# Performance work log

Hardware: AMD Instinct MI355X
Metric: run time of the kernel (lower is better)

## Reference

```python
import jax, jax.numpy as jnp
import numpy as np

B, S, D, H = 4, 2048, 256, 8
HD = D // H
SCALE = float(np.sqrt(HD))  # temperature = head_dim ** 0.5


def setup_inputs() -> dict:
    key = jax.random.key(0)
    ks = jax.random.split(key, 12)
    w = lambda k, shape: jax.random.normal(k, shape, dtype=jnp.float32) * 0.05
    x = jax.random.normal(ks[0], (B, S, D), dtype=jnp.float32)
    adj = jax.random.randint(ks[1], (B, S, S), 0, 2, dtype=jnp.int32)
    return {
        "x": x,
        "adj": adj,
        "w_qkv": w(ks[2], (3 * D, D)),
        "b_qkv": jnp.zeros((3 * D,), jnp.float32),
        "ln_g": jnp.ones((D,), jnp.float32),
        "ln_b": jnp.zeros((D,), jnp.float32),
        "w_fc": w(ks[3], (D, D)),
        "b_fc": jnp.zeros((D,), jnp.float32),
        "w_z": w(ks[4], (D, D)),
        "b_z": jnp.full((D,), -2.0, jnp.float32),  # init_bias fills w_z bias with -2
        "u_z": w(ks[5], (D, D)),
        "w_r": w(ks[6], (D, D)),
        "u_r": w(ks[7], (D, D)),
        "w_g": w(ks[8], (D, D)),
        "u_g": w(ks[9], (D, D)),
    }


def reference(x, adj, w_qkv, b_qkv, ln_g, ln_b, w_fc, b_fc,
              w_z, b_z, u_z, w_r, u_r, w_g, u_g):
    residual = x
    # LayerNorm (eps=1e-5, torch default)
    mu = jnp.mean(x, axis=-1, keepdims=True)
    var = jnp.var(x, axis=-1, keepdims=True)
    xn = (x - mu) / jnp.sqrt(var + 1e-5) * ln_g + ln_b
    # fused QKV projection -> (B*H, S, 3*HD), batch-major over (b, h)
    qkv = xn @ w_qkv.T + b_qkv                       # [B,S,3D]
    qkv = qkv.reshape(B, S, H, 3 * HD).transpose(0, 2, 1, 3).reshape(B * H, S, 3 * HD)
    q, k, v = jnp.split(qkv, 3, axis=-1)
    # masked scaled dot-product attention (full NxN scores, as in original)
    attn = jnp.einsum('nqd,nkd->nqk', q, k) / SCALE  # [B*H,S,S]
    adj_r = jnp.repeat(adj, H, axis=0)               # batch-major, matches attn layout
    attn = jnp.where(adj_r == 0, -jnp.inf, attn)
    attn = jax.nn.softmax(attn, axis=-1)
    out = jnp.einsum('nqk,nkd->nqd', attn, v)        # [B*H,S,HD]
    # Faithful replication of torch's view(n_head, batch, ...) applied to
    # batch-major data (an ordering quirk in the original module).
    out = out.reshape(H, B, S, HD).transpose(1, 2, 0, 3).reshape(B, S, D)
    y = jax.nn.relu(out @ w_fc.T + b_fc)
    # GRU gate: x=residual, y=attention branch
    z = jax.nn.sigmoid(y @ w_z.T + b_z + residual @ u_z.T)
    r = jax.nn.sigmoid(y @ w_r.T + residual @ u_r.T)
    h_hat = jnp.tanh(y @ w_g.T + (r * residual) @ u_g.T)
    return (1.0 - z) * residual + z * h_hat
```

## Files before the change

### kernel.cpp

```cpp
#include <hip/hip_runtime.h>
#include <hip/hip_bf16.h>
#include <math.h>

#define B_  4
#define S_  2048
#define D_  256
#define H_  8
#define HD_ 32
#define INV_SCALE 0.17677669529663687f

typedef short  bf16x8 __attribute__((ext_vector_type(8)));
typedef float  f32x4  __attribute__((ext_vector_type(4)));
typedef unsigned short ushort_t;
typedef unsigned int   uint_t;

__device__ __forceinline__ ushort_t f2b(float f) {
    union { float f; unsigned u; } v; v.f = f;
    unsigned r = (v.u + 0x7FFFu + ((v.u >> 16) & 1u)) >> 16;
    return (ushort_t)r;
}
__device__ __forceinline__ float b2f(ushort_t s) {
    return __uint_as_float((uint_t)s << 16);
}

__device__ __forceinline__ float wave_sum(float v) {
#pragma unroll
    for (int o = 32; o > 0; o >>= 1) v += __shfl_down(v, o, 64);
    return v;
}
__device__ __forceinline__ float block_sum256(float v, float* scr) {
    v = wave_sum(v);
    int lane = threadIdx.x & 63, wid = threadIdx.x >> 6;
    if (lane == 0) scr[wid] = v;
    __syncthreads();
    float r = scr[0] + scr[1] + scr[2] + scr[3];
    __syncthreads();
    return r;
}

#define WQ_SZ 196608
#define WS_SZ 65536
#define NB_ADJ 65536
#define NB_WC  2560
#define NB_LN  8192
__global__ __launch_bounds__(256)
void prep_kernel(const int* __restrict__ adj, uint_t* __restrict__ bits,
                 const float* __restrict__ w0, const float* __restrict__ w1,
                 const float* __restrict__ w2, const float* __restrict__ w3,
                 const float* __restrict__ w4, const float* __restrict__ w5,
                 const float* __restrict__ w6, const float* __restrict__ w7,
                 ushort_t* __restrict__ wout,
                 const float* __restrict__ x, const float* __restrict__ g,
                 const float* __restrict__ bb, ushort_t* __restrict__ xn_b) {
    __shared__ float scr[4];
    int blk = blockIdx.x, tid = threadIdx.x;
    if (blk < NB_ADJ) {
        size_t i = (size_t)blk * 256 + tid;
        unsigned long long m = __ballot(adj[i] != 0);
        int lane = tid & 63;
        size_t wbase = ((size_t)blk * 256 + (tid & ~63)) >> 5;
        if (lane == 0)  bits[wbase]     = (uint_t)m;
        if (lane == 32) bits[wbase + 1] = (uint_t)(m >> 32);
    } else if (blk < NB_ADJ + NB_WC) {
        int idx = (blk - NB_ADJ) * 256 + tid;
        const float* src; int o;
        if (idx < WQ_SZ) { src = w0; o = idx; }
        else {
            int j = idx - WQ_SZ, seg = j >> 16; o = j & (WS_SZ - 1);
            src = (seg == 0) ? w1 : (seg == 1) ? w2 : (seg == 2) ? w3 :
                  (seg == 3) ? w4 : (seg == 4) ? w5 : (seg == 5) ? w6 : w7;
        }
        int j  = o & 7;
        int l  = (o >> 3) & 15;
        int qd = (o >> 7) & 3;
        int ks = (o >> 9) & 7;
        int ct = o >> 12;
        wout[idx] = f2b(src[(ct * 16 + l) * 256 + ks * 32 + qd * 8 + j]);
    } else {
        size_t base = (size_t)(blk - NB_ADJ - NB_WC) * D_;
        float v  = x[base + tid];
        float mu = block_sum256(v, scr) * (1.0f / D_);
        float d  = v - mu;
        float var = block_sum256(d * d, scr) * (1.0f / D_);
        float rstd = rsqrtf(var + 1e-5f);
        xn_b[base + tid] = f2b(d * rstd * g[tid] + bb[tid]);
    }
}

__global__ __launch_bounds__(256)
void gemm_qkv(const ushort_t* __restrict__ A, const ushort_t* __restrict__ Wf,
              const float* __restrict__ bias, ushort_t* __restrict__ outb) {
    __shared__ ushort_t Sa[64][264];
    int tid = threadIdx.x;
    int wave = tid >> 6, lane = tid & 63, l = lane & 15, quad = lane >> 4;
    int wm = wave >> 1, wn = wave & 1;
    int m0 = blockIdx.y * 64, n0 = blockIdx.x * 64;
    {
        int row = tid >> 2, c0 = (tid & 3) * 64;
        const ushort_t* ap = A + (size_t)(m0 + row) * 256 + c0;
#pragma unroll
        for (int j = 0; j < 8; ++j)
            *(uint4*)&Sa[row][c0 + 8 * j] = ((const uint4*)ap)[j];
    }
    __syncthreads();

    bf16x8 af[2][8];
#pragma unroll
    for (int mt = 0; mt < 2; ++mt)
#pragma unroll
        for (int ks = 0; ks < 8; ++ks)
            af[mt][ks] = *(const bf16x8*)&Sa[wm * 32 + mt * 16 + l][ks * 32 + quad * 8];

    f32x4 acc[2][2];
#pragma unroll
    for (int i = 0; i < 2; ++i)
#pragma unroll
        for (int j = 0; j < 2; ++j) acc[i][j] = (f32x4){0.f, 0.f, 0.f, 0.f};

#pragma unroll
    for (int nt = 0; nt < 2; ++nt) {
        int ct = (n0 >> 4) + wn * 2 + nt;
        bf16x8 wfr[8];
#pragma unroll
        for (int ks = 0; ks < 8; ++ks)
            wfr[ks] = *(const bf16x8*)(Wf + (((size_t)ct * 8 + ks) * 64 + lane) * 8);
#pragma unroll
        for (int ks = 0; ks < 8; ++ks) {
            acc[0][nt] = __builtin_amdgcn_mfma_f32_16x16x32_bf16(af[0][ks], wfr[ks], acc[0][nt], 0, 0, 0);
            acc[1][nt] = __builtin_amdgcn_mfma_f32_16x16x32_bf16(af[1][ks], wfr[ks], acc[1][nt], 0, 0, 0);
        }
    }

    __syncthreads();
    ushort_t* So = &Sa[0][0];
#pragma unroll
    for (int nt = 0; nt < 2; ++nt) {
        int col = wn * 32 + nt * 16 + l;
        int gcol = n0 + col;
        float bv = bias[gcol];
        float qs = ((gcol % 96) < 32) ? INV_SCALE : 1.0f;
#pragma unroll
        for (int mt = 0; mt < 2; ++mt)
#pragma unroll
            for (int r = 0; r < 4; ++r) {
                int row = wm * 32 + mt * 16 + quad * 4 + r;
                So[row * 72 + col] = f2b((acc[mt][nt][r] + bv) * qs);
            }
    }
    __syncthreads();
    {
        int row = tid >> 2, seg = tid & 3;
        uint4 v0 = *(uint4*)&So[row * 72 + seg * 16];
        uint4 v1 = *(uint4*)&So[row * 72 + seg * 16 + 8];
        ushort_t* op = outb + (size_t)(m0 + row) * 768 + n0 + seg * 16;
        ((uint4*)op)[0] = v0;
        ((uint4*)op)[1] = v1;
    }
}

__global__ __launch_bounds__(256)
void fused_gate(const ushort_t* __restrict__ attn_b, const float* __restrict__ xf,
                const ushort_t* __restrict__ wfc, const ushort_t* __restrict__ wz,
                const ushort_t* __restrict__ uz, const ushort_t* __restrict__ wr,
                const ushort_t* __restrict__ ur, const ushort_t* __restrict__ wg,
                const ushort_t* __restrict__ ug, const float* __restrict__ bfc,
                const float* __restrict__ bz, float* __restrict__ out) {
    __shared__ ushort_t Sa[16][264];
    __shared__ ushort_t Sx[16][264];
    __shared__ ushort_t Sy[16][264];
    __shared__ ushort_t St[16][264];
    int tid = threadIdx.x;
    int wave = tid >> 6, lane = tid & 63, l = lane & 15, quad = lane >> 4;
    int m0 = blockIdx.x * 16;
    int colbase = wave * 64;

    {
        int row = tid >> 4, c0 = (tid & 15) * 16;
        const ushort_t* ap = attn_b + (size_t)(m0 + row) * 256 + c0;
        uint4 a0 = ((const uint4*)ap)[0];
        uint4 a1 = ((const uint4*)ap)[1];
        *(uint4*)&Sa[row][c0] = a0;
        *(uint4*)&Sa[row][c0 + 8] = a1;
        const float4* xp = (const float4*)(xf + (size_t)(m0 + row) * 256 + c0);
        float4 f0 = xp[0], f1 = xp[1], f2_ = xp[2], f3 = xp[3];
        union { __hip_bfloat162 h[4]; uint4 u; } p0, p1;
        p0.h[0] = __float22bfloat162_rn(make_float2(f0.x, f0.y));
        p0.h[1] = __float22bfloat162_rn(make_float2(f0.z, f0.w));
        p0.h[2] = __float22bfloat162_rn(make_float2(f1.x, f1.y));
        p0.h[3] = __float22bfloat162_rn(make_float2(f1.z, f1.w));
        p1.h[0] = __float22bfloat162_rn(make_float2(f2_.x, f2_.y));
        p1.h[1] = __float22bfloat162_rn(make_float2(f2_.z, f2_.w));
        p1.h[2] = __float22bfloat162_rn(make_float2(f3.x, f3.y));
        p1.h[3] = __float22bfloat162_rn(make_float2(f3.z, f3.w));
        *(uint4*)&Sx[row][c0]     = p0.u;
        *(uint4*)&Sx[row][c0 + 8] = p1.u;
    }
    __syncthreads();

    {
        bf16x8 af[8];
#pragma unroll
        for (int ks = 0; ks < 8; ++ks)
            af[ks] = *(const bf16x8*)&Sa[l][ks * 32 + quad * 8];
        f32x4 ya[4];
#pragma unroll
        for (int nt = 0; nt < 4; ++nt) ya[nt] = (f32x4){0.f, 0.f, 0.f, 0.f};
#pragma unroll
        for (int nt = 0; nt < 4; ++nt) {
            size_t fb = ((size_t)(wave * 4 + nt) * 8) * 512 + lane * 8;
#pragma unroll
            for (int ks = 0; ks < 8; ++ks) {
                bf16x8 wfr = *(const bf16x8*)(wfc + fb + ks * 512);
                ya[nt] = __builtin_amdgcn_mfma_f32_16x16x32_bf16(af[ks], wfr, ya[nt], 0, 0, 0);
            }
        }
#pragma unroll
        for (int nt = 0; nt < 4; ++nt) {
            int col = colbase + nt * 16 + l;
            float bv = bfc[col];
#pragma unroll
            for (int r = 0; r < 4; ++r)
                Sy[quad * 4 + r][col] = f2b(fmaxf(ya[nt][r] + bv, 0.0f));
        }
    }
    __syncthreads();

    f32x4 az[4], ar[4], ag[4];
#pragma unroll
    for (int nt = 0; nt < 4; ++nt) {
        az[nt] = (f32x4){0.f, 0.f, 0.f, 0.f};
        ar[nt] = (f32x4){0.f, 0.f, 0.f, 0.f};
        ag[nt] = (f32x4){0.f, 0.f, 0.f, 0.f};
    }
#pragma unroll
    for (int nt = 0; nt < 4; ++nt) {
        size_t fb = ((size_t)(wave * 4 + nt) * 8) * 512 + lane * 8;
#pragma unroll
        for (int ks = 0; ks < 8; ++ks) {
            bf16x8 fy = *(const bf16x8*)&Sy[l][ks * 32 + quad * 8];
            bf16x8 fx = *(const bf16x8*)&Sx[l][ks * 32 + quad * 8];
            bf16x8 fz  = *(const bf16x8*)(wz + fb + ks * 512);
            bf16x8 fuz = *(const bf16x8*)(uz + fb + ks * 512);
            bf16x8 fr  = *(const bf16x8*)(wr + fb + ks * 512);
            bf16x8 fur = *(const bf16x8*)(ur + fb + ks * 512);
            bf16x8 fg  = *(const bf16x8*)(wg + fb + ks * 512);
            az[nt] = __builtin_amdgcn_mfma_f32_16x16x32_bf16(fy, fz,  az[nt], 0, 0, 0);
            az[nt] = __builtin_amdgcn_mfma_f32_16x16x32_bf16(fx, fuz, az[nt], 0, 0, 0);
            ar[nt] = __builtin_amdgcn_mfma_f32_16x16x32_bf16(fy, fr,  ar[nt], 0, 0, 0);
            ar[nt] = __builtin_amdgcn_mfma_f32_16x16x32_bf16(fx, fur, ar[nt], 0, 0, 0);
            ag[nt] = __builtin_amdgcn_mfma_f32_16x16x32_bf16(fy, fg,  ag[nt], 0, 0, 0);
        }
    }
#pragma unroll
    for (int nt = 0; nt < 4; ++nt) {
        int col = colbase + nt * 16 + l;
        float bzv = bz[col];
#pragma unroll
        for (int r = 0; r < 4; ++r) {
            int row = quad * 4 + r;
            az[nt][r] = 1.0f / (1.0f + __expf(-(az[nt][r] + bzv)));
            float rr  = 1.0f / (1.0f + __expf(-ar[nt][r]));
            St[row][col] = f2b(rr * b2f(Sx[row][col]));
        }
    }
    __syncthreads();

    f32x4 fcc[4];
#pragma unroll
    for (int nt = 0; nt < 4; ++nt) fcc[nt] = (f32x4){0.f, 0.f, 0.f, 0.f};
#pragma unroll
    for (int nt = 0; nt < 4; ++nt) {
        size_t fb = ((size_t)(wave * 4 + nt) * 8) * 512 + lane * 8;
#pragma unroll
        for (int ks = 0; ks < 8; ++ks) {
            bf16x8 ft = *(const bf16x8*)&St[l][ks * 32 + quad * 8];
            bf16x8 fu = *(const bf16x8*)(ug + fb + ks * 512);
            fcc[nt] = __builtin_amdgcn_mfma_f32_16x16x32_bf16(ft, fu, fcc[nt], 0, 0, 0);
        }
    }
#pragma unroll
    for (int nt = 0; nt < 4; ++nt) {
        int col = colbase + nt * 16 + l;
#pragma unroll
        for (int r = 0; r < 4; ++r) {
            int row = quad * 4 + r;
            float v = ag[nt][r] + fcc[nt][r];
            float e = __expf(2.0f * v);
            float h = 1.0f - 2.0f / (e + 1.0f);
            float zz = az[nt][r];
            size_t idx = (size_t)(m0 + row) * 256 + col;
            out[idx] = (1.0f - zz) * xf[idx] + zz * h;
        }
    }
}

__global__ __launch_bounds__(256)
void attn_kernel(const ushort_t* __restrict__ qkvb, const uint_t* __restrict__ abits,
                 ushort_t* __restrict__ attn_b) {
    __shared__ ushort_t Ks[64][40];
    __shared__ ushort_t Vt[32][72];
    __shared__ ushort_t Ps[64][72];
    __shared__ uint_t  ab_sh[64][2];

    int tid = threadIdx.x;
    int wave = tid >> 6, lane = tid & 63, l = lane & 15, quad = lane >> 4;
    int q0 = blockIdx.x * 64;
    int n  = blockIdx.y;
    int b = n >> 3, h = n & 7;
    int bp = n & 3, hp = n >> 2;

    const ushort_t* base = qkvb + (size_t)b * S_ * 768 + h * 96;
    int myq = wave * 16 + l;

    bf16x8 qf = *(const bf16x8*)(base + (size_t)(q0 + myq) * 768 + quad * 8);

    f32x4 oacc[2];
    oacc[0] = (f32x4){0.f, 0.f, 0.f, 0.f};
    oacc[1] = (f32x4){0.f, 0.f, 0.f, 0.f};
    float lsum = 0.0f;

    int skey = tid >> 2, spart = tid & 3;
    int kcol = (spart * 8) ^ (((skey >> 3) & 1) << 3);
    int vcol = skey ^ (spart << 4);

    uint4 kv = *(const uint4*)(base + (size_t)skey * 768 + 32 + spart * 8);
    uint4 vv = *(const uint4*)(base + (size_t)skey * 768 + 64 + spart * 8);
    uint_t aw = 0;
    if (tid < 128)
        aw = abits[((size_t)b * S_ + q0 + (tid >> 1)) * 64 + (tid & 1)];

    for (int k0 = 0; k0 < S_; k0 += 64) {
        uint4 kc = kv, vc = vv; uint_t ac = aw;
        if (k0 + 64 < S_) {
            kv = *(const uint4*)(base + (size_t)(k0 + 64 + skey) * 768 + 32 + spart * 8);
            vv = *(const uint4*)(base + (size_t)(k0 + 64 + skey) * 768 + 64 + spart * 8);
            if (tid < 128)
                aw = abits[((size_t)b * S_ + q0 + (tid >> 1)) * 64 + ((k0 + 64) >> 5) + (tid & 1)];
        }
        __syncthreads();
        *(uint4*)&Ks[skey][kcol] = kc;
        {
            const ushort_t* vs = (const ushort_t*)&vc;
#pragma unroll
            for (int i = 0; i < 8; ++i) Vt[spart * 8 + i][vcol] = vs[i];
        }
        if (tid < 128) ab_sh[tid >> 1][tid & 1] = ac;
        __syncthreads();

        uint_t aw0 = ab_sh[myq][0], aw1 = ab_sh[myq][1];

#pragma unroll
        for (int t4 = 0; t4 < 4; ++t4) {
            bf16x8 kf = *(const bf16x8*)&Ks[t4 * 16 + l][(quad * 8) ^ ((l >> 3) << 3)];
            f32x4 z = (f32x4){0.f, 0.f, 0.f, 0.f};
            f32x4 sc = __builtin_amdgcn_mfma_f32_16x16x32_bf16(kf, qf, z, 0, 0, 0);
            uint_t w = (t4 & 2) ? aw1 : aw0;
            uint_t wq = w >> ((t4 & 1) * 16 + quad * 4);
            float p[4];
#pragma unroll
            for (int r = 0; r < 4; ++r) {
                uint_t mneg = 0u - ((wq >> r) & 1u);
                float e = __expf(sc[r]);
                p[r] = __uint_as_float(__float_as_uint(e) & mneg);
                lsum += p[r];
            }
            union { __hip_bfloat162 b2[2]; uint2 u2; } pk;
            pk.b2[0] = __float22bfloat162_rn(make_float2(p[0], p[1]));
            pk.b2[1] = __float22bfloat162_rn(make_float2(p[2], p[3]));
            *(uint2*)&Ps[myq][t4 * 16 + quad * 4] = pk.u2;
        }

#pragma unroll
        for (int ks = 0; ks < 2; ++ks) {
            bf16x8 pf = *(const bf16x8*)&Ps[wave * 16 + l][ks * 32 + quad * 8];
#pragma unroll
            for (int mt = 0; mt < 2; ++mt) {
                int vc2 = (ks * 32 + quad * 8) ^ ((mt * 2 + (l >> 3)) << 4);
                bf16x8 vf = *(const bf16x8*)&Vt[mt * 16 + l][vc2];
                oacc[mt] = __builtin_amdgcn_mfma_f32_16x16x32_bf16(vf, pf, oacc[mt], 0, 0, 0);
            }
        }
    }

    lsum += __shfl_xor(lsum, 16, 64);
    lsum += __shfl_xor(lsum, 32, 64);
    float linv = 1.0f / lsum;

    __syncthreads();
    ushort_t* Ost = &Ks[0][0];
#pragma unroll
    for (int mt = 0; mt < 2; ++mt)
#pragma unroll
        for (int r = 0; r < 4; ++r)
            Ost[myq * 40 + mt * 16 + quad * 4 + r] = f2b(oacc[mt][r] * linv);
    __syncthreads();
    {
        int q = tid >> 2, part = tid & 3;
        uint4 v = *(uint4*)&Ost[q * 40 + part * 8];
        *(uint4*)&attn_b[((size_t)(bp * S_ + q0 + q)) * 256 + hp * 32 + part * 8] = v;
    }
}

extern "C" void kernel_launch(void* const* d_in, const int* in_sizes, int n_in,
                              void* d_out, int out_size, void* d_ws, size_t ws_size,
                              hipStream_t stream) {
    const float* x     = (const float*)d_in[0];
    const int*   adj   = (const int*)d_in[1];
    const float* w_qkv = (const float*)d_in[2];
    const float* b_qkv = (const float*)d_in[3];
    const float* ln_g  = (const float*)d_in[4];
    const float* ln_b  = (const float*)d_in[5];
    const float* w_fc  = (const float*)d_in[6];
    const float* b_fc  = (const float*)d_in[7];
    const float* w_z   = (const float*)d_in[8];
    const float* b_z   = (const float*)d_in[9];
    const float* u_z   = (const float*)d_in[10];
    const float* w_r   = (const float*)d_in[11];
    const float* u_r   = (const float*)d_in[12];
    const float* w_g   = (const float*)d_in[13];
    const float* u_g   = (const float*)d_in[14];
    float* out = (float*)d_out;

    const size_t TOK  = (size_t)B_ * S_;
    const size_t TOKD = TOK * D_;
    ushort_t* xn_b   = (ushort_t*)d_ws;
    ushort_t* qkv_b  = xn_b + TOKD;
    ushort_t* attn_b = qkv_b + TOK * 768;
    ushort_t* wb     = attn_b + TOKD;
    uint_t*   bits   = (uint_t*)(wb + WQ_SZ + 7 * WS_SZ);

    ushort_t* wq_b  = wb;
    ushort_t* wfc_b = wb + WQ_SZ;
    ushort_t* wz_b  = wfc_b + WS_SZ;
    ushort_t* uz_b  = wz_b + WS_SZ;
    ushort_t* wr_b  = uz_b + WS_SZ;
    ushort_t* ur_b  = wr_b + WS_SZ;
    ushort_t* wg_b  = ur_b + WS_SZ;
    ushort_t* ug_b  = wg_b + WS_SZ;

    prep_kernel<<<NB_ADJ + NB_WC + NB_LN, 256, 0, stream>>>(
        adj, bits, w_qkv, w_fc, w_z, u_z, w_r, u_r, w_g, u_g, wb,
        x, ln_g, ln_b, xn_b);

    gemm_qkv<<<dim3(12, 128), 256, 0, stream>>>(xn_b, wq_b, b_qkv, qkv_b);

    attn_kernel<<<dim3(S_ / 64, B_ * H_), 256, 0, stream>>>(qkv_b, bits, attn_b);

    fused_gate<<<512, 256, 0, stream>>>(
        attn_b, x, wfc_b, wz_b, uz_b, wr_b, ur_b, wg_b, ug_b, b_fc, b_z, out);
}
```

Measured before the change: 247.1 us.

## Pre-transpose V in QKV GEMM, double-buffer attention tiles, fold log2e into Q

The QKV GEMM epilogue now also writes V transposed per head into a separate workspace buffer. The attention kernel can then load V rows with vectorized loads instead of scattering scalar transposes into shared memory. K and V tiles are double-buffered, so each iteration needs one barrier instead of two, and mask bits are read straight from global memory into registers instead of through shared memory. The Q scale now includes log2(e), which lets exp2f replace __expf. The cost is an extra V write in the GEMM epilogue plus an extra barrier there.

After: 248.9 us. About the same (+0.7%).

```diff
diff --git a/kernel.cpp b/kernel.cpp
--- a/kernel.cpp
+++ b/kernel.cpp
@@ -7,7 +7,7 @@
 #define D_  256
 #define H_  8
 #define HD_ 32
-#define INV_SCALE 0.17677669529663687f
+#define QSCALE 0.25504175929589786f
 
 typedef short  bf16x8 __attribute__((ext_vector_type(8)));
 typedef float  f32x4  __attribute__((ext_vector_type(4)));
@@ -89,7 +89,8 @@
 
 __global__ __launch_bounds__(256)
 void gemm_qkv(const ushort_t* __restrict__ A, const ushort_t* __restrict__ Wf,
-              const float* __restrict__ bias, ushort_t* __restrict__ outb) {
+              const float* __restrict__ bias, ushort_t* __restrict__ outb,
+              ushort_t* __restrict__ vT) {
     __shared__ ushort_t Sa[64][264];
     int tid = threadIdx.x;
     int wave = tid >> 6, lane = tid & 63, l = lane & 15, quad = lane >> 4;
@@ -138,7 +139,7 @@
         int col = wn * 32 + nt * 16 + l;
         int gcol = n0 + col;
         float bv = bias[gcol];
-        float qs = ((gcol % 96) < 32) ? INV_SCALE : 1.0f;
+        float qs = ((gcol % 96) < 32) ? QSCALE : 1.0f;
 #pragma unroll
         for (int mt = 0; mt < 2; ++mt)
 #pragma unroll
@@ -155,6 +156,33 @@
         ushort_t* op = outb + (size_t)(m0 + row) * 768 + n0 + seg * 16;
         ((uint4*)op)[0] = v0;
         ((uint4*)op)[1] = v1;
+    }
+
+    int vs = n0 % 96;
+    if (vs != 0) {
+        int vloc = (vs == 64) ? 0 : 32;
+        int h  = (n0 + vloc) / 96;
+        int b  = m0 >> 11;
+        int s0 = m0 & (S_ - 1);
+        ushort_t* vstage = &Sa[0][0] + 8192;
+        {
+            int c = tid & 31, seg = tid >> 5;
+            ushort_t tmp[8];
+#pragma unroll
+            for (int i = 0; i < 8; ++i)
+                tmp[i] = So[(seg * 8 + i) * 72 + vloc + c];
+            uint_t u[4];
+#pragma unroll
+            for (int i = 0; i < 4; ++i)
+                u[i] = (uint_t)tmp[2 * i] | ((uint_t)tmp[2 * i + 1] << 16);
+            *(uint4*)&vstage[c * 72 + seg * 8] = make_uint4(u[0], u[1], u[2], u[3]);
+        }
+        __syncthreads();
+        {
+            int d = tid >> 3, tseg = tid & 7;
+            uint4 v = *(uint4*)&vstage[d * 72 + tseg * 8];
+            *(uint4*)&vT[((size_t)(b * 8 + h) * 32 + d) * S_ + s0 + tseg * 8] = v;
+        }
     }
 }
 
@@ -295,12 +323,11 @@
 }
 
 __global__ __launch_bounds__(256)
-void attn_kernel(const ushort_t* __restrict__ qkvb, const uint_t* __restrict__ abits,
-                 ushort_t* __restrict__ attn_b) {
-    __shared__ ushort_t Ks[64][40];
-    __shared__ ushort_t Vt[32][72];
+void attn_kernel(const ushort_t* __restrict__ qkvb, const ushort_t* __restrict__ vT,
+                 const uint_t* __restrict__ abits, ushort_t* __restrict__ attn_b) {
+    __shared__ ushort_t Ks[2][64][40];
+    __shared__ ushort_t Vt[2][32][72];
     __shared__ ushort_t Ps[64][72];
-    __shared__ uint_t  ab_sh[64][2];
 
     int tid = threadIdx.x;
     int wave = tid >> 6, lane = tid & 63, l = lane & 15, quad = lane >> 4;
@@ -321,37 +348,29 @@
 
     int skey = tid >> 2, spart = tid & 3;
     int kcol = (spart * 8) ^ (((skey >> 3) & 1) << 3);
-    int vcol = skey ^ (spart << 4);
+    int vd = tid >> 3, vk = (tid & 7) * 8;
+    const ushort_t* vptr = vT + ((size_t)n * 32 + vd) * S_ + vk;
+    const uint_t* aptr = abits + ((size_t)b * S_ + q0 + myq) * 64;
 
     uint4 kv = *(const uint4*)(base + (size_t)skey * 768 + 32 + spart * 8);
-    uint4 vv = *(const uint4*)(base + (size_t)skey * 768 + 64 + spart * 8);
-    uint_t aw = 0;
-    if (tid < 128)
-        aw = abits[((size_t)b * S_ + q0 + (tid >> 1)) * 64 + (tid & 1)];
+    uint4 vv = *(const uint4*)(vptr);
+    uint2 aw = *(const uint2*)(aptr);
 
     for (int k0 = 0; k0 < S_; k0 += 64) {
-        uint4 kc = kv, vc = vv; uint_t ac = aw;
+        int cur = (k0 >> 6) & 1;
+        *(uint4*)&Ks[cur][skey][kcol] = kv;
+        *(uint4*)&Vt[cur][vd][vk] = vv;
+        uint_t aw0 = aw.x, aw1 = aw.y;
         if (k0 + 64 < S_) {
             kv = *(const uint4*)(base + (size_t)(k0 + 64 + skey) * 768 + 32 + spart * 8);
-            vv = *(const uint4*)(base + (size_t)(k0 + 64 + skey) * 768 + 64 + spart * 8);
-            if (tid < 128)
-                aw = abits[((size_t)b * S_ + q0 + (tid >> 1)) * 64 + ((k0 + 64) >> 5) + (tid & 1)];
+            vv = *(const uint4*)(vptr + k0 + 64);
+            aw = *(const uint2*)(aptr + ((k0 + 64) >> 5));
         }
         __syncthreads();
-        *(uint4*)&Ks[skey][kcol] = kc;
-        {
-            const ushort_t* vs = (const ushort_t*)&vc;
-#pragma unroll
-            for (int i = 0; i < 8; ++i) Vt[spart * 8 + i][vcol] = vs[i];
-        }
-        if (tid < 128) ab_sh[tid >> 1][tid & 1] = ac;
-        __syncthreads();
-
-        uint_t aw0 = ab_sh[myq][0], aw1 = ab_sh[myq][1];
 
 #pragma unroll
         for (int t4 = 0; t4 < 4; ++t4) {
-            bf16x8 kf = *(const bf16x8*)&Ks[t4 * 16 + l][(quad * 8) ^ ((l >> 3) << 3)];
+            bf16x8 kf = *(const bf16x8*)&Ks[cur][t4 * 16 + l][(quad * 8) ^ ((l >> 3) << 3)];
             f32x4 z = (f32x4){0.f, 0.f, 0.f, 0.f};
             f32x4 sc = __builtin_amdgcn_mfma_f32_16x16x32_bf16(kf, qf, z, 0, 0, 0);
             uint_t w = (t4 & 2) ? aw1 : aw0;
@@ -360,7 +379,7 @@
 #pragma unroll
             for (int r = 0; r < 4; ++r) {
                 uint_t mneg = 0u - ((wq >> r) & 1u);
-                float e = __expf(sc[r]);
+                float e = exp2f(sc[r]);
                 p[r] = __uint_as_float(__float_as_uint(e) & mneg);
                 lsum += p[r];
             }
@@ -375,8 +394,7 @@
             bf16x8 pf = *(const bf16x8*)&Ps[wave * 16 + l][ks * 32 + quad * 8];
 #pragma unroll
             for (int mt = 0; mt < 2; ++mt) {
-                int vc2 = (ks * 32 + quad * 8) ^ ((mt * 2 + (l >> 3)) << 4);
-                bf16x8 vf = *(const bf16x8*)&Vt[mt * 16 + l][vc2];
+                bf16x8 vf = *(const bf16x8*)&Vt[cur][mt * 16 + l][ks * 32 + quad * 8];
                 oacc[mt] = __builtin_amdgcn_mfma_f32_16x16x32_bf16(vf, pf, oacc[mt], 0, 0, 0);
             }
         }
@@ -387,7 +405,7 @@
     float linv = 1.0f / lsum;
 
     __syncthreads();
-    ushort_t* Ost = &Ks[0][0];
+    ushort_t* Ost = &Ks[0][0][0];
 #pragma unroll
     for (int mt = 0; mt < 2; ++mt)
 #pragma unroll
@@ -428,6 +446,7 @@
     ushort_t* attn_b = qkv_b + TOK * 768;
     ushort_t* wb     = attn_b + TOKD;
     uint_t*   bits   = (uint_t*)(wb + WQ_SZ + 7 * WS_SZ);
+    ushort_t* vTb    = (ushort_t*)(bits + (size_t)B_ * S_ * S_ / 32);
 
     ushort_t* wq_b  = wb;
     ushort_t* wfc_b = wb + WQ_SZ;
@@ -442,9 +461,9 @@
         adj, bits, w_qkv, w_fc, w_z, u_z, w_r, u_r, w_g, u_g, wb,
         x, ln_g, ln_b, xn_b);
 
-    gemm_qkv<<<dim3(12, 128), 256, 0, stream>>>(xn_b, wq_b, b_qkv, qkv_b);
-
-    attn_kernel<<<dim3(S_ / 64, B_ * H_), 256, 0, stream>>>(qkv_b, bits, attn_b);
+    gemm_qkv<<<dim3(12, 128), 256, 0, stream>>>(xn_b, wq_b, b_qkv, qkv_b, vTb);
+
+    attn_kernel<<<dim3(S_ / 64, B_ * H_), 256, 0, stream>>>(qkv_b, vTb, bits, attn_b);
 
     fused_gate<<<512, 256, 0, stream>>>(
         attn_b, x, wfc_b, wz_b, uz_b, wr_b, ur_b, wg_b, ug_b, b_fc, b_z, out);
```
